# Kernel optimization log

Measured on AMD Instinct MI355X. Metric: run time of the kernel, lower is better.

Reference implementation:

```python
import jax, jax.numpy as jnp
import numpy as np

K = 1024
H = 128

def setup_inputs() -> dict:
    key = jax.random.key(0)
    ks = jax.random.split(key, 11)
    s = lambda fan_in: 1.0 / np.sqrt(fan_in)
    # coord_mlp: Linear(H, H//2) -> GELU -> Linear(H//2, 2)
    cW1 = jax.random.uniform(ks[0], (H, H // 2), minval=-s(H), maxval=s(H))
    cb1 = jax.random.uniform(ks[1], (H // 2,), minval=-s(H), maxval=s(H))
    cW2 = jax.random.uniform(ks[2], (H // 2, 2), minval=-s(H // 2), maxval=s(H // 2))
    cb2 = jax.random.uniform(ks[3], (2,), minval=-s(H // 2), maxval=s(H // 2))
    # edge_mlp: Linear(2H, H) -> GELU -> Linear(H, H//2) -> GELU -> Linear(H//2, 1)
    eW1 = jax.random.uniform(ks[4], (2 * H, H), minval=-s(2 * H), maxval=s(2 * H))
    eb1 = jax.random.uniform(ks[5], (H,), minval=-s(2 * H), maxval=s(2 * H))
    eW2 = jax.random.uniform(ks[6], (H, H // 2), minval=-s(H), maxval=s(H))
    eb2 = jax.random.uniform(ks[7], (H // 2,), minval=-s(H), maxval=s(H))
    eW3 = jax.random.uniform(ks[8], (H // 2, 1), minval=-s(H // 2), maxval=s(H // 2))
    eb3 = jax.random.uniform(ks[9], (1,), minval=-s(H // 2), maxval=s(H // 2))
    z_s = jax.random.normal(ks[10], (K, H), dtype=jnp.float32)
    return {"z_s": z_s, "cW1": cW1, "cb1": cb1, "cW2": cW2, "cb2": cb2,
            "eW1": eW1, "eb1": eb1, "eW2": eW2, "eb2": eb2, "eW3": eW3, "eb3": eb3}

def reference(z_s, cW1, cb1, cW2, cb2, eW1, eb1, eW2, eb2, eW3, eb3):
    gelu = lambda x: jax.nn.gelu(x, approximate=False)  # torch default GELU is exact erf form
    # coords: [k, 2]
    coords_pred = gelu(z_s @ cW1 + cb1) @ cW2 + cb2
    # edge first layer: cat([zi, zj]) @ eW1 == zi @ eW1[:H] + zj @ eW1[H:]
    # (same math as the broadcast-concat, without materializing [k, k, 2H])
    pi = z_s @ eW1[:H]   # [k, H]
    pj = z_s @ eW1[H:]   # [k, H]
    h1 = gelu(pi[:, None, :] + pj[None, :, :] + eb1)   # [k, k, H]
    h2 = gelu(h1 @ eW2 + eb2)                          # [k, k, H//2]
    adj_logits = (h2 @ eW3 + eb3)[..., 0]              # [k, k]
    adj_logits = (adj_logits + adj_logits.T) / 2.0
    return (coords_pred, adj_logits)
```

## Files before the change

kernel.cpp:

```cpp
#include <hip/hip_runtime.h>
#include <hip/hip_fp16.h>


#define KN 1024
#define HN 128

typedef float  floatx4 __attribute__((ext_vector_type(4)));
typedef _Float16 half8v __attribute__((ext_vector_type(8)));

__device__ __forceinline__ float gelu_f(float x) {
    float x2 = x * x;
    float t  = fmaf(x2, -0.1029434f, -2.3022087f);
    float e  = __builtin_amdgcn_exp2f(x * t);
    return x * __builtin_amdgcn_rcpf(e + 1.0f);
}

__device__ __forceinline__ unsigned int gelu2u(unsigned int xu) {
    __half2 x  = __builtin_bit_cast(__half2, xu);
    __half2 x2 = __hmul2(x, x);
    __half2 t  = __hfma2(x2, __float2half2_rn(-0.1029434f),
                             __float2half2_rn(-2.3022087f));
    __half2 e  = h2exp2(__hmul2(x, t));
    __half2 r  = h2rcp(__hadd2(e, __float2half2_rn(1.0f)));
    return __builtin_bit_cast(unsigned int, __hmul2(x, r));
}

__global__ __launch_bounds__(256) void prep_kernel(
    const float* __restrict__ z,   const float* __restrict__ cW1,
    const float* __restrict__ cb1, const float* __restrict__ cW2,
    const float* __restrict__ cb2, const float* __restrict__ eW1,
    const float* __restrict__ eb1, const float* __restrict__ eW2,
    _Float16* __restrict__ pi_h,   _Float16* __restrict__ pj_h,
    _Float16* __restrict__ w2T,    float* __restrict__ coords ) {
    __shared__ float z8[8][128];
    __shared__ float c1s[8][64];
    const int tid = threadIdx.x;
    const int r0  = blockIdx.x * 8;

    if (blockIdx.x < 32) {
        int e = blockIdx.x * 256 + tid;
        w2T[e] = (_Float16)eW2[(e & 127) * 64 + (e >> 7)];
    }

#pragma unroll
    for (int s = 0; s < 4; ++s) {
        int e = tid + 256 * s;
        z8[e >> 7][e & 127] = z[r0 * HN + e];
    }
    __syncthreads();

    const int col = tid & 127, which = tid >> 7;
    const float* w = eW1 + which * HN * HN + col;
    float acc8[8] = {0.f, 0.f, 0.f, 0.f, 0.f, 0.f, 0.f, 0.f};
    for (int k = 0; k < HN; ++k) {
        float wv = w[k * HN];
#pragma unroll
        for (int r = 0; r < 8; ++r) acc8[r] = fmaf(z8[r][k], wv, acc8[r]);
    }
    if (which == 0) {
        float b = eb1[col];
#pragma unroll
        for (int r = 0; r < 8; ++r)
            pi_h[(r0 + r) * HN + col] = (_Float16)(acc8[r] + b);
    } else {
#pragma unroll
        for (int r = 0; r < 8; ++r)
            pj_h[(r0 + r) * HN + col] = (_Float16)acc8[r];
    }

#pragma unroll
    for (int s = 0; s < 2; ++s) {
        int task = tid + 256 * s;
        int row = task >> 6, mid = task & 63;
        float a = cb1[mid];
        for (int k = 0; k < HN; ++k) a = fmaf(z8[row][k], cW1[k * 64 + mid], a);
        c1s[row][mid] = gelu_f(a);
    }
    __syncthreads();
    if (tid < 16) {
        int row = tid >> 1, o = tid & 1;
        float a = cb2[o];
#pragma unroll 8
        for (int m = 0; m < 64; ++m) a = fmaf(c1s[row][m], cW2[m * 2 + o], a);
        coords[(r0 + row) * 2 + o] = a;
    }
}

__global__ __launch_bounds__(256, 4) void edge_kernel(
    const _Float16* __restrict__ pi_h, const _Float16* __restrict__ pj_h,
    const _Float16* __restrict__ w2T,  const float* __restrict__ eb2,
    const float* __restrict__ eW3,     const float* __restrict__ eb3,
    float* __restrict__ out_adj) {
    __shared__ __align__(16) _Float16 pi_s[32][136];
    __shared__ __align__(16) _Float16 pj_s[32][136];
    const int i0 = blockIdx.y * 32, j0 = blockIdx.x * 32;
    const int tid = threadIdx.x;

    const unsigned int* piu = (const unsigned int*)pi_h;
    const unsigned int* pju = (const unsigned int*)pj_h;
#pragma unroll
    for (int s = 0; s < 8; ++s) {
        int e = tid + 256 * s;
        int r = e >> 6, c2 = e & 63;
        *reinterpret_cast<unsigned int*>(&pi_s[r][c2 * 2]) = piu[(i0 + r) * 64 + c2];
        *reinterpret_cast<unsigned int*>(&pj_s[r][c2 * 2]) = pju[(j0 + r) * 64 + c2];
    }

    const int lane = tid & 63;
    const int wave = tid >> 6;
    const int lrow = lane & 15;
    const int lhi  = lane >> 4;

    half8v bfrag[4][4];
#pragma unroll
    for (int q = 0; q < 4; ++q)
#pragma unroll
        for (int c = 0; c < 4; ++c)
            bfrag[q][c] = *reinterpret_cast<const half8v*>(
                &w2T[(c * 16 + lrow) * HN + q * 32 + lhi * 8]);
    float eb2_l[4], w3_l[4];
#pragma unroll
    for (int c = 0; c < 4; ++c) {
        eb2_l[c] = eb2[c * 16 + lrow];
        w3_l[c]  = eW3[c * 16 + lrow];
    }
    const float b3 = eb3[0];
    __syncthreads();

    for (int t = 0; t < 16; ++t) {
        const int g  = wave * 16 + t;
        const int iL = g >> 1;
        const int jL = ((g & 1) << 4) + lrow;

        floatx4 acc[4];
#pragma unroll
        for (int c = 0; c < 4; ++c) acc[c] = (floatx4){0.f, 0.f, 0.f, 0.f};

#pragma unroll
        for (int q = 0; q < 4; ++q) {
            const int kb = q * 32 + lhi * 8;
            half8v a = *reinterpret_cast<const half8v*>(&pi_s[iL][kb]);
            half8v b = *reinterpret_cast<const half8v*>(&pj_s[jL][kb]);
            uint4 su = __builtin_bit_cast(uint4, a + b);
            uint4 gu;
            gu.x = gelu2u(su.x);
            gu.y = gelu2u(su.y);
            gu.z = gelu2u(su.z);
            gu.w = gelu2u(su.w);
            half8v af = __builtin_bit_cast(half8v, gu);
#pragma unroll
            for (int c = 0; c < 4; ++c)
                acc[c] = __builtin_amdgcn_mfma_f32_16x16x32_f16(
                    af, bfrag[q][c], acc[c], 0, 0, 0);
        }

        float tv[4];
#pragma unroll
        for (int m = 0; m < 4; ++m) {
            float s = 0.f;
#pragma unroll
            for (int c = 0; c < 4; ++c)
                s = fmaf(gelu_f(acc[c][m] + eb2_l[c]), w3_l[c], s);
            s += __shfl_xor(s, 1);
            s += __shfl_xor(s, 2);
            s += __shfl_xor(s, 4);
            s += __shfl_xor(s, 8);
            tv[m] = s + b3;
        }
        if (lrow == 0) {
#pragma unroll
            for (int m = 0; m < 4; ++m) {
                int p = g * 16 + lhi * 4 + m;
                out_adj[(size_t)(i0 + (p >> 5)) * KN + (j0 + (p & 31))] = tv[m];
            }
        }
    }
}

__global__ __launch_bounds__(256) void sym_kernel(float* __restrict__ adj) {
    int idx = blockIdx.x * 256 + threadIdx.x;
    int i = idx >> 10, j = idx & 1023;
    if (j < i) return;
    float a = adj[i * KN + j];
    float b = adj[j * KN + i];
    float m = 0.5f * (a + b);
    adj[i * KN + j] = m;
    adj[j * KN + i] = m;
}

extern "C" void kernel_launch(void* const* d_in, const int* in_sizes, int n_in,
                              void* d_out, int out_size, void* d_ws, size_t ws_size,
                              hipStream_t stream) {
    const float* z   = (const float*)d_in[0];
    const float* cW1 = (const float*)d_in[1];
    const float* cb1 = (const float*)d_in[2];
    const float* cW2 = (const float*)d_in[3];
    const float* cb2 = (const float*)d_in[4];
    const float* eW1 = (const float*)d_in[5];
    const float* eb1 = (const float*)d_in[6];
    const float* eW2 = (const float*)d_in[7];
    const float* eb2 = (const float*)d_in[8];
    const float* eW3 = (const float*)d_in[9];
    const float* eb3 = (const float*)d_in[10];

    float* out = (float*)d_out;
    _Float16* pi_h = (_Float16*)d_ws;
    _Float16* pj_h = pi_h + KN * HN;
    _Float16* w2T  = pj_h + KN * HN;

    prep_kernel<<<128, 256, 0, stream>>>(z, cW1, cb1, cW2, cb2, eW1, eb1, eW2,
                                         pi_h, pj_h, w2T, out);

    dim3 gridB(32, 32);
    edge_kernel<<<gridB, 256, 0, stream>>>(pi_h, pj_h, w2T, eb2, eW3, eb3,
                                           out + 2048);

    sym_kernel<<<4096, 256, 0, stream>>>(out + 2048);
}
```

Baseline: 87.72 us.

## Stage eW2 fragments in swizzled LDS and retile edge kernel to 32x16 blocks

```diff
diff --git a/kernel.cpp b/kernel.cpp
--- a/kernel.cpp
+++ b/kernel.cpp
@@ -86,38 +86,50 @@
     }
 }
 
-__global__ __launch_bounds__(256, 4) void edge_kernel(
+__global__ __launch_bounds__(512, 7) void edge_kernel(
     const _Float16* __restrict__ pi_h, const _Float16* __restrict__ pj_h,
     const _Float16* __restrict__ w2T,  const float* __restrict__ eb2,
     const float* __restrict__ eW3,     const float* __restrict__ eb3,
     float* __restrict__ out_adj) {
-    __shared__ __align__(16) _Float16 pi_s[32][136];
-    __shared__ __align__(16) _Float16 pj_s[32][136];
-    const int i0 = blockIdx.y * 32, j0 = blockIdx.x * 32;
+    __shared__ __align__(16) unsigned int pi_s[32 * 64];
+    __shared__ __align__(16) unsigned int pj_s[16 * 64];
+    __shared__ __align__(16) unsigned int w2_s[64 * 64];
+    const int i0 = blockIdx.y * 32, j0 = blockIdx.x * 16;
     const int tid = threadIdx.x;
 
     const unsigned int* piu = (const unsigned int*)pi_h;
     const unsigned int* pju = (const unsigned int*)pj_h;
+    const unsigned int* w2u = (const unsigned int*)w2T;
+
+#pragma unroll
+    for (int s = 0; s < 4; ++s) {
+        int e = tid + 512 * s;
+        int r = e >> 6;
+        pi_s[e ^ ((r & 7) << 2)] = piu[(i0 + r) * 64 + (e & 63)];
+    }
+#pragma unroll
+    for (int s = 0; s < 2; ++s) {
+        int e = tid + 512 * s;
+        int r = e >> 6;
+        pj_s[e ^ ((r & 7) << 2)] = pju[(j0 + r) * 64 + (e & 63)];
+    }
 #pragma unroll
     for (int s = 0; s < 8; ++s) {
-        int e = tid + 256 * s;
-        int r = e >> 6, c2 = e & 63;
-        *reinterpret_cast<unsigned int*>(&pi_s[r][c2 * 2]) = piu[(i0 + r) * 64 + c2];
-        *reinterpret_cast<unsigned int*>(&pj_s[r][c2 * 2]) = pju[(j0 + r) * 64 + c2];
+        int e = tid + 512 * s;
+        int r = e >> 6;
+        w2_s[e ^ ((r & 7) << 2)] = w2u[e];
     }
 
     const int lane = tid & 63;
     const int wave = tid >> 6;
     const int lrow = lane & 15;
     const int lhi  = lane >> 4;
-
-    half8v bfrag[4][4];
-#pragma unroll
-    for (int q = 0; q < 4; ++q)
-#pragma unroll
-        for (int c = 0; c < 4; ++c)
-            bfrag[q][c] = *reinterpret_cast<const half8v*>(
-                &w2T[(c * 16 + lrow) * HN + q * 32 + lhi * 8]);
+    const int lhi4 = lhi << 2;
+    const int swzJ = (lrow & 7) << 2;
+
+    const unsigned int* pjrow  = &pj_s[lrow << 6];
+    const unsigned int* w2base = &w2_s[lrow << 6];
+
     float eb2_l[4], w3_l[4];
 #pragma unroll
     for (int c = 0; c < 4; ++c) {
@@ -127,10 +139,11 @@
     const float b3 = eb3[0];
     __syncthreads();
 
-    for (int t = 0; t < 16; ++t) {
-        const int g  = wave * 16 + t;
-        const int iL = g >> 1;
-        const int jL = ((g & 1) << 4) + lrow;
+#pragma unroll
+    for (int t = 0; t < 4; ++t) {
+        const int iL = (wave << 2) + t;
+        const unsigned int* pirow = &pi_s[iL << 6];
+        const int swzI = (iL & 7) << 2;
 
         floatx4 acc[4];
 #pragma unroll
@@ -138,9 +151,9 @@
 
 #pragma unroll
         for (int q = 0; q < 4; ++q) {
-            const int kb = q * 32 + lhi * 8;
-            half8v a = *reinterpret_cast<const half8v*>(&pi_s[iL][kb]);
-            half8v b = *reinterpret_cast<const half8v*>(&pj_s[jL][kb]);
+            const int ko = (q << 4) + lhi4;
+            half8v a = *reinterpret_cast<const half8v*>(&pirow[ko ^ swzI]);
+            half8v b = *reinterpret_cast<const half8v*>(&pjrow[ko ^ swzJ]);
             uint4 su = __builtin_bit_cast(uint4, a + b);
             uint4 gu;
             gu.x = gelu2u(su.x);
@@ -148,10 +161,14 @@
             gu.z = gelu2u(su.z);
             gu.w = gelu2u(su.w);
             half8v af = __builtin_bit_cast(half8v, gu);
-#pragma unroll
-            for (int c = 0; c < 4; ++c)
+            const int kw = ko ^ swzJ;
+#pragma unroll
+            for (int c = 0; c < 4; ++c) {
+                half8v bf = *reinterpret_cast<const half8v*>(
+                    &w2base[(c << 10) + kw]);
                 acc[c] = __builtin_amdgcn_mfma_f32_16x16x32_f16(
-                    af, bfrag[q][c], acc[c], 0, 0, 0);
+                    af, bf, acc[c], 0, 0, 0);
+            }
         }
 
         float tv[4];
@@ -168,11 +185,9 @@
             tv[m] = s + b3;
         }
         if (lrow == 0) {
-#pragma unroll
-            for (int m = 0; m < 4; ++m) {
-                int p = g * 16 + lhi * 4 + m;
-                out_adj[(size_t)(i0 + (p >> 5)) * KN + (j0 + (p & 31))] = tv[m];
-            }
+            float4 v = make_float4(tv[0], tv[1], tv[2], tv[3]);
+            *reinterpret_cast<float4*>(
+                &out_adj[(size_t)(i0 + iL) * KN + j0 + lhi4]) = v;
         }
     }
 }
@@ -211,8 +226,8 @@
     prep_kernel<<<128, 256, 0, stream>>>(z, cW1, cb1, cW2, cb2, eW1, eb1, eW2,
                                          pi_h, pj_h, w2T, out);
 
-    dim3 gridB(32, 32);
-    edge_kernel<<<gridB, 256, 0, stream>>>(pi_h, pj_h, w2T, eb2, eW3, eb3,
+    dim3 gridB(64, 32);
+    edge_kernel<<<gridB, 512, 0, stream>>>(pi_h, pj_h, w2T, eb2, eW3, eb3,
                                            out + 2048);
 
     sym_kernel<<<4096, 256, 0, stream>>>(out + 2048);
```

After: 82.85 us. -5.5%, faster.
